# Kernel tuning notes

Hardware: AMD Instinct MI355X
Metric: run time of the kernel (lower is better)

Reference implementation:

```python
import jax, jax.numpy as jnp
import numpy as np

N_NODES = 50000
N_EDGES = 800000
HIDDEN = 128
BN_EPS = 1e-5


def setup_inputs() -> dict:
    key = jax.random.key(0)
    ks = jax.random.split(key, 4)
    x = jax.random.normal(ks[0], (N_NODES, HIDDEN), dtype=jnp.float32)
    edge_index = jax.random.randint(ks[1], (2, N_EDGES), 0, N_NODES, dtype=jnp.int64)
    scale = 1.0 / np.sqrt(HIDDEN)
    W1 = jax.random.normal(ks[2], (HIDDEN, HIDDEN), dtype=jnp.float32) * scale
    b1 = jnp.zeros((HIDDEN,), dtype=jnp.float32)
    W2 = jax.random.normal(ks[3], (HIDDEN, HIDDEN), dtype=jnp.float32) * scale
    b2 = jnp.zeros((HIDDEN,), dtype=jnp.float32)
    gamma = jnp.ones((HIDDEN,), dtype=jnp.float32)
    beta = jnp.zeros((HIDDEN,), dtype=jnp.float32)
    return {"x": x, "edge_index": edge_index, "W1": W1, "b1": b1,
            "W2": W2, "b2": b2, "gamma": gamma, "beta": beta}


def reference(x, edge_index, W1, b1, W2, b2, gamma, beta):
    # GINConv (eps=0): h_i = MLP( x_i + sum_{(j->i) in E} x_j )
    src = edge_index[0]
    dst = edge_index[1]
    agg = jax.ops.segment_sum(x[src], dst, num_segments=x.shape[0])  # [N, H]
    h = x + agg
    # 2-layer MLP: Linear -> ReLU -> Linear
    h = jnp.maximum(h @ W1 + b1, 0.0)
    h = h @ W2 + b2
    # BatchNorm1d over node dimension (training-mode batch statistics)
    mean = jnp.mean(h, axis=0)
    var = jnp.var(h, axis=0)
    h = (h - mean) * jax.lax.rsqrt(var + BN_EPS) * gamma + beta
    # add_activation=False (default): no ReLU. Dropout in eval mode: identity.
    return h
```

## Files before the change

kernel.cpp:

```cpp
#include <hip/hip_runtime.h>

typedef unsigned int u32;
typedef unsigned short u16;
typedef __attribute__((ext_vector_type(8))) short short8;
typedef __attribute__((ext_vector_type(4))) float f32x4;

static constexpr int NN = 50000;
static constexpr int NE = 800000;
static constexpr int HH = 128;
static constexpr int NB1 = (NN + 1023) / 1024;
static constexpr int NBK = 196;
static constexpr int EPB = 8192;
static constexpr int NEB = (NE + EPB - 1) / EPB;

__device__ __forceinline__ u32 bf16r(float f) {
  u32 u = __builtin_bit_cast(u32, f);
  return (u + 0x7FFFu + ((u >> 16) & 1u)) >> 16;
}
__device__ __forceinline__ u32 pk2(float lo, float hi) { return bf16r(lo) | (bf16r(hi) << 16); }
__device__ __forceinline__ float bl(u32 p) { return __builtin_bit_cast(float, p << 16); }
__device__ __forceinline__ float bh(u32 p) { return __builtin_bit_cast(float, p & 0xFFFF0000u); }

__global__ __launch_bounds__(256) void prep_kernel(const float4* __restrict__ x,
                                                   uint4* __restrict__ x16,
                                                   const float* __restrict__ W1,
                                                   u16* __restrict__ w1t,
                                                   const float* __restrict__ W2,
                                                   u16* __restrict__ w2t,
                                                   float* __restrict__ stats,
                                                   const int* __restrict__ ei,
                                                   int* __restrict__ hist2d) {
  __shared__ int hist[NBK];
  const int b = blockIdx.x, t = threadIdx.x;
  if (b < 3125) {
    const int i = b * 256 + t;
    const float4 a = x[2 * i];
    const float4 c = x[2 * i + 1];
    uint4 o;
    o.x = pk2(a.x, a.y);
    o.y = pk2(a.z, a.w);
    o.z = pk2(c.x, c.y);
    o.w = pk2(c.z, c.w);
    x16[i] = o;
  } else if (b < 3189) {
    const int o = (b - 3125) * 256 + t;
    const int n = o >> 7, k = o & 127;
    w1t[o] = (u16)bf16r(W1[k * 128 + n]);
  } else if (b < 3253) {
    const int o = (b - 3189) * 256 + t;
    const int n = o >> 7, k = o & 127;
    w2t[o] = (u16)bf16r(W2[k * 128 + n]);
  } else if (b == 3253) {
    stats[t] = 0.f;
  } else {
    const int hb = b - 3254;
    for (int i = t; i < NBK; i += 256) hist[i] = 0;
    __syncthreads();
    const int e0 = hb * EPB;
    const int e1 = min(e0 + EPB, NE);
    for (int e = e0 + t; e < e1; e += 256) atomicAdd(&hist[ei[NE + e] >> 8], 1);
    __syncthreads();
    for (int i = t; i < NBK; i += 256) hist2d[hb * NBK + i] = hist[i];
  }
}

__global__ __launch_bounds__(256) void ph3_kernel(const int* __restrict__ ei,
                                                  const int* __restrict__ hist2d,
                                                  u32* __restrict__ packed) {
  __shared__ int cur[NBK];
  __shared__ int tot[256];
  const int b = blockIdx.x, t = threadIdx.x;
  int total = 0, partial = 0;
  if (t < NBK) {
    for (int bb = 0; bb < NEB; ++bb) {
      const int v = hist2d[bb * NBK + t];
      total += v;
      if (bb < b) partial += v;
    }
  }
  tot[t] = total;
  __syncthreads();
  for (int off = 1; off < 256; off <<= 1) {
    const int add = (t >= off) ? tot[t - off] : 0;
    __syncthreads();
    tot[t] += add;
    __syncthreads();
  }
  if (t < NBK) cur[t] = (t ? tot[t - 1] : 0) + partial;
  __syncthreads();
  const int e0 = b * EPB;
  const int e1 = min(e0 + EPB, NE);
  for (int e = e0 + t; e < e1; e += 256) {
    const int s = ei[e];
    const int d = ei[NE + e];
    const int pos = atomicAdd(&cur[d >> 8], 1);
    packed[pos] = (u32)s | ((u32)(d & 255) << 16);
  }
}

__global__ __launch_bounds__(256) void ph4_kernel(const int* __restrict__ hist2d,
                                                  const u32* __restrict__ packed,
                                                  int* __restrict__ offs,
                                                  int* __restrict__ srcl) {
  __shared__ int hist[256];
  __shared__ int scn[256];
  __shared__ int sb[2];
  const int b = blockIdx.x, t = threadIdx.x;
  int total = 0;
  if (t < NBK)
    for (int bb = 0; bb < NEB; ++bb) total += hist2d[bb * NBK + t];
  scn[t] = total;
  __syncthreads();
  for (int off = 1; off < 256; off <<= 1) {
    const int add = (t >= off) ? scn[t - off] : 0;
    __syncthreads();
    scn[t] += add;
    __syncthreads();
  }
  if (t == b) {
    sb[0] = b ? scn[b - 1] : 0;
    sb[1] = scn[b];
  }
  __syncthreads();
  const int base = sb[0];
  const int cnt = sb[1] - base;

  hist[t] = 0;
  __syncthreads();
  for (int i = t; i < cnt; i += 256) atomicAdd(&hist[packed[base + i] >> 16], 1);
  __syncthreads();
  scn[t] = hist[t];
  __syncthreads();
  for (int off = 1; off < 256; off <<= 1) {
    const int add = (t >= off) ? scn[t - off] : 0;
    __syncthreads();
    scn[t] += add;
    __syncthreads();
  }
  const int excl = t ? scn[t - 1] : 0;
  const int node = b * 256 + t;
  if (node < NN) offs[node] = base + excl;
  if (b == NBK - 1 && t == 0) offs[NN] = NE;
  __syncthreads();
  hist[t] = excl;
  __syncthreads();
  for (int i = t; i < cnt; i += 256) {
    const u32 p = packed[base + i];
    const int r = atomicAdd(&hist[p >> 16], 1);
    srcl[base + r] = (int)(p & 0xFFFFu);
  }
}

__global__ __launch_bounds__(256) void gather16_kernel(const u32* __restrict__ x16,
                                                       const int* __restrict__ offs,
                                                       const int* __restrict__ srcl,
                                                       u32* __restrict__ h0) {
  const int qw = (blockIdx.x * 256 + threadIdx.x) >> 4;
  const int l16 = threadIdx.x & 15;
  const int nqw = gridDim.x * 16;
  const uint4* x4 = reinterpret_cast<const uint4*>(x16);
  for (int node = qw; node < NN; node += nqw) {
    const uint4 sv = x4[(size_t)node * 16 + l16];
    float a0 = bl(sv.x), a1 = bh(sv.x), a2 = bl(sv.y), a3 = bh(sv.y);
    float a4 = bl(sv.z), a5 = bh(sv.z), a6 = bl(sv.w), a7 = bh(sv.w);
    const int beg = offs[node], end = offs[node + 1];
    int e = beg;
    for (; e + 8 <= end; e += 8) {
      int s[8];
#pragma unroll
      for (int j = 0; j < 8; ++j) s[j] = srcl[e + j];
      uint4 v[8];
#pragma unroll
      for (int j = 0; j < 8; ++j) v[j] = x4[(size_t)s[j] * 16 + l16];
#pragma unroll
      for (int j = 0; j < 8; ++j) {
        a0 += bl(v[j].x); a1 += bh(v[j].x);
        a2 += bl(v[j].y); a3 += bh(v[j].y);
        a4 += bl(v[j].z); a5 += bh(v[j].z);
        a6 += bl(v[j].w); a7 += bh(v[j].w);
      }
    }
    for (; e < end; ++e) {
      const uint4 v = x4[(size_t)srcl[e] * 16 + l16];
      a0 += bl(v.x); a1 += bh(v.x);
      a2 += bl(v.y); a3 += bh(v.y);
      a4 += bl(v.z); a5 += bh(v.z);
      a6 += bl(v.w); a7 += bh(v.w);
    }
    uint4 o;
    o.x = pk2(a0, a1);
    o.y = pk2(a2, a3);
    o.z = pk2(a4, a5);
    o.w = pk2(a6, a7);
    reinterpret_cast<uint4*>(h0)[(size_t)node * 16 + l16] = o;
  }
}

__global__ __launch_bounds__(256) void fused_mlp_kernel(const u16* __restrict__ h0,
                                                        const u16* __restrict__ w1t,
                                                        const float* __restrict__ b1,
                                                        const u16* __restrict__ w2t,
                                                        const float* __restrict__ b2,
                                                        u32* __restrict__ h2,
                                                        float* __restrict__ stats,
                                                        int nchunk) {
  __shared__ __align__(16) u16 hs[16][136];
  __shared__ float sstats[256];
  const int t = threadIdx.x;
  const int w = t >> 6;
  const int lane = t & 63;
  const int lhi = lane >> 4, llo = lane & 15;
  sstats[t] = 0.f;

  short8 w1f[2][4], w2f[2][4];
  float4 bs1[2], bs2[2];
#pragma unroll
  for (int c = 0; c < 2; ++c) {
    const int ct = 2 * w + c;
#pragma unroll
    for (int kb = 0; kb < 4; ++kb) {
      w1f[c][kb] = *reinterpret_cast<const short8*>(w1t + (size_t)(16 * ct + llo) * 128 + kb * 32 + lhi * 8);
      w2f[c][kb] = *reinterpret_cast<const short8*>(w2t + (size_t)(16 * ct + llo) * 128 + kb * 32 + lhi * 8);
    }
    bs1[c] = *reinterpret_cast<const float4*>(b1 + ct * 16 + lhi * 4);
    bs2[c] = *reinterpret_cast<const float4*>(b2 + ct * 16 + lhi * 4);
  }
  __syncthreads();

  for (int ch = blockIdx.x; ch < nchunk; ch += gridDim.x) {
    const int row0 = ch * 16;

    const u16* arow = h0 + (size_t)(row0 + llo) * 128;
    short8 afr[4];
#pragma unroll
    for (int kb = 0; kb < 4; ++kb)
      afr[kb] = *reinterpret_cast<const short8*>(arow + kb * 32 + lhi * 8);

    f32x4 acc0 = {0.f, 0.f, 0.f, 0.f};
    f32x4 acc1 = {0.f, 0.f, 0.f, 0.f};
#pragma unroll
    for (int kb = 0; kb < 4; ++kb) {
      acc0 = __builtin_amdgcn_mfma_f32_16x16x32_bf16(w1f[0][kb], afr[kb], acc0, 0, 0, 0);
      acc1 = __builtin_amdgcn_mfma_f32_16x16x32_bf16(w1f[1][kb], afr[kb], acc1, 0, 0, 0);
    }

#pragma unroll
    for (int c = 0; c < 2; ++c) {
      const int ct = 2 * w + c;
      const f32x4 a = c ? acc1 : acc0;
      const float4 bb = c ? bs1[1] : bs1[0];
      const float v0 = fmaxf(a[0] + bb.x, 0.f);
      const float v1 = fmaxf(a[1] + bb.y, 0.f);
      const float v2 = fmaxf(a[2] + bb.z, 0.f);
      const float v3 = fmaxf(a[3] + bb.w, 0.f);
      u32* dst = reinterpret_cast<u32*>(&hs[llo][ct * 16 + lhi * 4]);
      dst[0] = pk2(v0, v1);
      dst[1] = pk2(v2, v3);
    }
    __syncthreads();

    short8 af2[4];
#pragma unroll
    for (int kb = 0; kb < 4; ++kb)
      af2[kb] = *reinterpret_cast<const short8*>(&hs[llo][kb * 32 + lhi * 8]);

    f32x4 dcc0 = {0.f, 0.f, 0.f, 0.f};
    f32x4 dcc1 = {0.f, 0.f, 0.f, 0.f};
#pragma unroll
    for (int kb = 0; kb < 4; ++kb) {
      dcc0 = __builtin_amdgcn_mfma_f32_16x16x32_bf16(w2f[0][kb], af2[kb], dcc0, 0, 0, 0);
      dcc1 = __builtin_amdgcn_mfma_f32_16x16x32_bf16(w2f[1][kb], af2[kb], dcc1, 0, 0, 0);
    }
    __syncthreads();

#pragma unroll
    for (int c = 0; c < 2; ++c) {
      const int ct = 2 * w + c;
      const f32x4 a = c ? dcc1 : dcc0;
      const float4 bb = c ? bs2[1] : bs2[0];
      float v0 = a[0] + bb.x;
      float v1 = a[1] + bb.y;
      float v2 = a[2] + bb.z;
      float v3 = a[3] + bb.w;
      u32* op = h2 + (size_t)(row0 + llo) * 64 + ct * 8 + lhi * 2;
      op[0] = pk2(v0, v1);
      op[1] = pk2(v2, v3);
      float q0 = v0 * v0, q1 = v1 * v1, q2 = v2 * v2, q3 = v3 * v3;
#pragma unroll
      for (int m = 1; m < 16; m <<= 1) {
        v0 += __shfl_xor(v0, m, 64); v1 += __shfl_xor(v1, m, 64);
        v2 += __shfl_xor(v2, m, 64); v3 += __shfl_xor(v3, m, 64);
        q0 += __shfl_xor(q0, m, 64); q1 += __shfl_xor(q1, m, 64);
        q2 += __shfl_xor(q2, m, 64); q3 += __shfl_xor(q3, m, 64);
      }
      if (llo == 0) {
        const int cb = ct * 16 + lhi * 4;
        atomicAdd(&sstats[cb + 0], v0); atomicAdd(&sstats[cb + 1], v1);
        atomicAdd(&sstats[cb + 2], v2); atomicAdd(&sstats[cb + 3], v3);
        atomicAdd(&sstats[128 + cb + 0], q0); atomicAdd(&sstats[128 + cb + 1], q1);
        atomicAdd(&sstats[128 + cb + 2], q2); atomicAdd(&sstats[128 + cb + 3], q3);
      }
    }
  }
  __syncthreads();
  atomicAdd(&stats[t], sstats[t]);
}

__global__ __launch_bounds__(256) void bn16_kernel(const u32* __restrict__ h2,
                                                   const float* __restrict__ stats,
                                                   const float* __restrict__ gamma,
                                                   const float* __restrict__ beta,
                                                   float* __restrict__ out, float invn) {
  __shared__ float scale_s[128], shift_s[128];
  const int t = threadIdx.x;
  if (t < 128) {
    const float mean = stats[t] * invn;
    float var = fmaf(-mean, mean, stats[128 + t] * invn);
    var = fmaxf(var, 0.f);
    const float rs = rsqrtf(var + 1e-5f);
    const float sc = gamma[t] * rs;
    scale_s[t] = sc;
    shift_s[t] = fmaf(-mean, sc, beta[t]);
  }
  __syncthreads();
  int i = blockIdx.x * 256 + t;
  const int stride = gridDim.x * 256;
  for (; i < NN * 64; i += stride) {
    const int c = (i & 63) * 2;
    const u32 p = h2[i];
    float2 o;
    o.x = fmaf(bl(p), scale_s[c + 0], shift_s[c + 0]);
    o.y = fmaf(bh(p), scale_s[c + 1], shift_s[c + 1]);
    *reinterpret_cast<float2*>(out + 2 * (size_t)i) = o;
  }
}

__global__ void zero_stats_kernel(float* __restrict__ stats) { stats[threadIdx.x] = 0.f; }

__global__ __launch_bounds__(256) void zero_int_kernel(int* __restrict__ p, int n) {
  int i = blockIdx.x * blockDim.x + threadIdx.x;
  const int stride = gridDim.x * blockDim.x;
  for (; i < n; i += stride) p[i] = 0;
}

__global__ __launch_bounds__(256) void count_kernel(const int* __restrict__ ei,
                                                    int* __restrict__ cnt) {
  const int e = blockIdx.x * blockDim.x + threadIdx.x;
  if (e < NE) atomicAdd(&cnt[ei[NE + e]], 1);
}

__global__ __launch_bounds__(256) void scan1_kernel(const int* __restrict__ cnt,
                                                    int* __restrict__ offs,
                                                    int* __restrict__ partials) {
  __shared__ int tsum[256];
  const int b = blockIdx.x, t = threadIdx.x;
  const int base = b * 1024 + t * 4;
  int v[4];
  int s = 0;
#pragma unroll
  for (int j = 0; j < 4; ++j) {
    const int idx = base + j;
    v[j] = (idx < NN) ? cnt[idx] : 0;
    s += v[j];
  }
  tsum[t] = s;
  __syncthreads();
#pragma unroll
  for (int off = 1; off < 256; off <<= 1) {
    const int add = (t >= off) ? tsum[t - off] : 0;
    __syncthreads();
    tsum[t] += add;
    __syncthreads();
  }
  int excl = (t ? tsum[t - 1] : 0);
#pragma unroll
  for (int j = 0; j < 4; ++j) {
    const int idx = base + j;
    if (idx < NN) offs[idx] = excl;
    excl += v[j];
  }
  if (t == 255) partials[b] = tsum[255];
}

__global__ void scan2_kernel(int* __restrict__ partials, int nb) {
  const int t = threadIdx.x;
  int v = (t < nb) ? partials[t] : 0;
#pragma unroll
  for (int off = 1; off < 64; off <<= 1) {
    const int n = __shfl_up(v, off, 64);
    if (t >= off) v += n;
  }
  int excl = __shfl_up(v, 1, 64);
  if (t == 0) excl = 0;
  if (t < nb) partials[t] = excl;
}

__global__ __launch_bounds__(256) void scan3_kernel(int* __restrict__ offs,
                                                    int* __restrict__ cursor,
                                                    const int* __restrict__ partials) {
  const int b = blockIdx.x;
  const int add = partials[b];
#pragma unroll
  for (int j = 0; j < 4; ++j) {
    const int idx = b * 1024 + threadIdx.x + j * 256;
    if (idx < NN) {
      const int o = offs[idx] + add;
      offs[idx] = o;
      cursor[idx] = o;
    }
  }
  if (b == 0 && threadIdx.x == 0) offs[NN] = NE;
}

__global__ __launch_bounds__(256) void fill_kernel(const int* __restrict__ ei,
                                                   int* __restrict__ cursor,
                                                   int* __restrict__ srcl) {
  const int e = blockIdx.x * blockDim.x + threadIdx.x;
  if (e >= NE) return;
  const int s = ei[e];
  const int d = ei[NE + e];
  const int pos = atomicAdd(&cursor[d], 1);
  srcl[pos] = s;
}

__global__ __launch_bounds__(256) void gather_kernel(const float* __restrict__ x,
                                                     const int* __restrict__ offs,
                                                     const int* __restrict__ srcl,
                                                     float* __restrict__ out) {
  const int wave = (blockIdx.x * 256 + threadIdx.x) >> 6;
  const int lane = threadIdx.x & 63;
  const int nwaves = gridDim.x * 4;
  for (int node = wave; node < NN; node += nwaves) {
    float2 acc = *reinterpret_cast<const float2*>(x + (size_t)node * HH + lane * 2);
    const int beg = offs[node], end = offs[node + 1];
    for (int e = beg; e < end; ++e) {
      const int s = srcl[e];
      const float2 v = *reinterpret_cast<const float2*>(x + (size_t)s * HH + lane * 2);
      acc.x += v.x;
      acc.y += v.y;
    }
    *reinterpret_cast<float2*>(out + (size_t)node * HH + lane * 2) = acc;
  }
}

__global__ __launch_bounds__(256) void copy_x_kernel(const float4* __restrict__ x,
                                                     float4* __restrict__ h, int n4) {
  int i = blockIdx.x * blockDim.x + threadIdx.x;
  const int stride = gridDim.x * blockDim.x;
  for (; i < n4; i += stride) h[i] = x[i];
}

__global__ __launch_bounds__(256) void scatter_kernel(const float* __restrict__ x,
                                                      const int* __restrict__ ei,
                                                      float* __restrict__ h) {
  const long long tid = (long long)blockIdx.x * blockDim.x + threadIdx.x;
  const int e = (int)(tid >> 5);
  if (e >= NE) return;
  const int c = (int)(tid & 31);
  const int s = ei[e];
  const int d = ei[NE + e];
  const float4 v = *reinterpret_cast<const float4*>(x + (size_t)s * HH + c * 4);
  float* dp = h + (size_t)d * HH + c * 4;
  atomicAdd(dp + 0, v.x);
  atomicAdd(dp + 1, v.y);
  atomicAdd(dp + 2, v.z);
  atomicAdd(dp + 3, v.w);
}

template <bool RELU>
__global__ __launch_bounds__(256, 2) void gemm128_kernel(const float* in,
                                                         const float* __restrict__ W,
                                                         const float* __restrict__ bias,
                                                         float* out,
                                                         int nrows, int nchunks) {
  __shared__ float Ws[128][128];
  __shared__ float rows_s[32][128];
  const int t = threadIdx.x;
  for (int i = t; i < 128 * 128 / 4; i += 256) {
    reinterpret_cast<float4*>(&Ws[0][0])[i] = reinterpret_cast<const float4*>(W)[i];
  }
  const int col4 = (t & 31) * 4;
  const int rowg = (t >> 5) * 4;
  const float4 b4 = *reinterpret_cast<const float4*>(bias + col4);

  for (int chunk = blockIdx.x; chunk < nchunks; chunk += gridDim.x) {
    const int row0 = chunk * 32;
    __syncthreads();
    for (int i = t; i < 1024; i += 256) {
      const int rr = i >> 5, cc = (i & 31) * 4;
      const int grow = row0 + rr;
      float4 v = make_float4(0.f, 0.f, 0.f, 0.f);
      if (grow < nrows) v = *reinterpret_cast<const float4*>(in + (size_t)grow * HH + cc);
      *reinterpret_cast<float4*>(&rows_s[rr][cc]) = v;
    }
    __syncthreads();

    float acc[4][4] = {};
#pragma unroll 4
    for (int k = 0; k < 128; k += 4) {
      float4 a[4];
#pragma unroll
      for (int r = 0; r < 4; ++r) a[r] = *reinterpret_cast<const float4*>(&rows_s[rowg + r][k]);
#pragma unroll
      for (int kk = 0; kk < 4; ++kk) {
        const float4 wv = *reinterpret_cast<const float4*>(&Ws[k + kk][col4]);
#pragma unroll
        for (int r = 0; r < 4; ++r) {
          const float av = (&a[r].x)[kk];
          acc[r][0] = fmaf(av, wv.x, acc[r][0]);
          acc[r][1] = fmaf(av, wv.y, acc[r][1]);
          acc[r][2] = fmaf(av, wv.z, acc[r][2]);
          acc[r][3] = fmaf(av, wv.w, acc[r][3]);
        }
      }
    }

#pragma unroll
    for (int r = 0; r < 4; ++r) {
      const int grow = row0 + rowg + r;
      if (grow < nrows) {
        float4 o;
        o.x = acc[r][0] + b4.x;
        o.y = acc[r][1] + b4.y;
        o.z = acc[r][2] + b4.z;
        o.w = acc[r][3] + b4.w;
        if (RELU) {
          o.x = fmaxf(o.x, 0.f); o.y = fmaxf(o.y, 0.f);
          o.z = fmaxf(o.z, 0.f); o.w = fmaxf(o.w, 0.f);
        }
        *reinterpret_cast<float4*>(out + (size_t)grow * HH + col4) = o;
      }
    }
  }
}

__global__ __launch_bounds__(256) void col_stats_kernel(const float* __restrict__ h,
                                                        float* __restrict__ stats, int nrows) {
  __shared__ float ssum[256], ssq[256];
  const int t = threadIdx.x;
  const int col = t & 127;
  const int half = t >> 7;
  float s = 0.f, q = 0.f;
  for (int r = blockIdx.x * 2 + half; r < nrows; r += gridDim.x * 2) {
    const float v = h[(size_t)r * HH + col];
    s += v;
    q = fmaf(v, v, q);
  }
  ssum[t] = s;
  ssq[t] = q;
  __syncthreads();
  if (t < 128) {
    atomicAdd(&stats[col], ssum[t] + ssum[t + 128]);
    atomicAdd(&stats[128 + col], ssq[t] + ssq[t + 128]);
  }
}

__global__ __launch_bounds__(256) void bn_apply_kernel(float* __restrict__ h,
                                                       const float* __restrict__ stats,
                                                       const float* __restrict__ gamma,
                                                       const float* __restrict__ beta,
                                                       int n4, float invn) {
  __shared__ float scale_s[128], shift_s[128];
  const int t = threadIdx.x;
  if (t < 128) {
    const float mean = stats[t] * invn;
    float var = fmaf(-mean, mean, stats[128 + t] * invn);
    var = fmaxf(var, 0.f);
    const float rs = rsqrtf(var + 1e-5f);
    const float sc = gamma[t] * rs;
    scale_s[t] = sc;
    shift_s[t] = fmaf(-mean, sc, beta[t]);
  }
  __syncthreads();
  float4* h4 = reinterpret_cast<float4*>(h);
  int i = blockIdx.x * blockDim.x + threadIdx.x;
  const int stride = gridDim.x * blockDim.x;
  for (; i < n4; i += stride) {
    const int c = (i & 31) * 4;
    float4 v = h4[i];
    v.x = fmaf(v.x, scale_s[c + 0], shift_s[c + 0]);
    v.y = fmaf(v.y, scale_s[c + 1], shift_s[c + 1]);
    v.z = fmaf(v.z, scale_s[c + 2], shift_s[c + 2]);
    v.w = fmaf(v.w, scale_s[c + 3], shift_s[c + 3]);
    h4[i] = v;
  }
}

extern "C" void kernel_launch(void* const* d_in, const int* in_sizes, int n_in,
                              void* d_out, int out_size, void* d_ws, size_t ws_size,
                              hipStream_t stream) {
  const float* x = (const float*)d_in[0];
  const int* ei = (const int*)d_in[1];
  const float* W1 = (const float*)d_in[2];
  const float* b1 = (const float*)d_in[3];
  const float* W2 = (const float*)d_in[4];
  const float* b2 = (const float*)d_in[5];
  const float* gamma = (const float*)d_in[6];
  const float* beta = (const float*)d_in[7];
  float* out = (float*)d_out;

  auto AL = [](size_t v) { return (v + 255) & ~(size_t)255; };
  const size_t offs_b = AL((size_t)(NN + 1) * 4);
  const size_t srcl_b = AL((size_t)NE * 4);
  const size_t packed_b = AL((size_t)NE * 4);
  const size_t h2d_b = AL((size_t)NEB * NBK * 4);
  const size_t stats_b = AL(256 * 4);
  const size_t x16_b = AL((size_t)NN * HH * 2);
  const size_t wt_b = AL((size_t)128 * 128 * 2);
  const size_t need_A = offs_b + srcl_b + packed_b + h2d_b + stats_b + x16_b + 2 * wt_b;

  const size_t cnt_b = AL((size_t)NN * 4);
  const size_t part_b = AL(64 * 4);
  const size_t need_B = offs_b + cnt_b + part_b + srcl_b + stats_b;

  if (ws_size >= need_A) {
    char* p = (char*)d_ws;
    int* offs = (int*)p;       p += offs_b;
    int* srcl = (int*)p;       p += srcl_b;
    u32* packed = (u32*)p;     p += packed_b;
    int* hist2d = (int*)p;     p += h2d_b;
    float* stats = (float*)p;  p += stats_b;
    u16* x16 = (u16*)p;        p += x16_b;
    u16* w1t = (u16*)p;        p += wt_b;
    u16* w2t = (u16*)p;

    prep_kernel<<<3254 + NEB, 256, 0, stream>>>((const float4*)x, (uint4*)x16, W1, w1t,
                                                W2, w2t, stats, ei, hist2d);
    ph3_kernel<<<NEB, 256, 0, stream>>>(ei, hist2d, packed);
    ph4_kernel<<<NBK, 256, 0, stream>>>(hist2d, packed, offs, srcl);

    gather16_kernel<<<2048, 256, 0, stream>>>((const u32*)x16, offs, srcl, (u32*)d_out);

    const int nchunk = NN / 16;
    u32* h2 = (u32*)x16;
    fused_mlp_kernel<<<512, 256, 0, stream>>>((const u16*)d_out, w1t, b1, w2t, b2,
                                              h2, stats, nchunk);
    bn16_kernel<<<2048, 256, 0, stream>>>(h2, stats, gamma, beta, out, 1.0f / NN);
  } else if (ws_size >= need_B) {
    char* p = (char*)d_ws;
    int* offs = (int*)p;      p += offs_b;
    int* cnt = (int*)p;       p += cnt_b;
    int* partials = (int*)p;  p += part_b;
    int* srcl = (int*)p;      p += srcl_b;
    float* stats = (float*)p;

    zero_int_kernel<<<64, 256, 0, stream>>>(cnt, NN);
    count_kernel<<<(NE + 255) / 256, 256, 0, stream>>>(ei, cnt);
    scan1_kernel<<<NB1, 256, 0, stream>>>(cnt, offs, partials);
    scan2_kernel<<<1, 64, 0, stream>>>(partials, NB1);
    scan3_kernel<<<NB1, 256, 0, stream>>>(offs, cnt, partials);
    fill_kernel<<<(NE + 255) / 256, 256, 0, stream>>>(ei, cnt, srcl);
    gather_kernel<<<1024, 256, 0, stream>>>(x, offs, srcl, out);

    zero_stats_kernel<<<1, 256, 0, stream>>>(stats);
    const int nchunks = (NN + 31) / 32;
    gemm128_kernel<true><<<512, 256, 0, stream>>>(out, W1, b1, out, NN, nchunks);
    gemm128_kernel<false><<<512, 256, 0, stream>>>(out, W2, b2, out, NN, nchunks);
    col_stats_kernel<<<1024, 256, 0, stream>>>(out, stats, NN);
    bn_apply_kernel<<<2048, 256, 0, stream>>>(out, stats, gamma, beta, NN * HH / 4, 1.0f / NN);
  } else {
    float* stats = (float*)d_ws;
    copy_x_kernel<<<2048, 256, 0, stream>>>((const float4*)x, (float4*)out, NN * HH / 4);
    const long long sthreads = (long long)NE * 32;
    scatter_kernel<<<(int)((sthreads + 255) / 256), 256, 0, stream>>>(x, ei, out);
    zero_stats_kernel<<<1, 256, 0, stream>>>(stats);
    const int nchunks = (NN + 31) / 32;
    gemm128_kernel<true><<<512, 256, 0, stream>>>(out, W1, b1, out, NN, nchunks);
    gemm128_kernel<false><<<512, 256, 0, stream>>>(out, W2, b2, out, NN, nchunks);
    col_stats_kernel<<<1024, 256, 0, stream>>>(out, stats, NN);
    bn_apply_kernel<<<2048, 256, 0, stream>>>(out, stats, gamma, beta, NN * HH / 4, 1.0f / NN);
  }
}
```

Measured before the change: 131.5 us.

## Fuse per-bucket CSR sort into gather kernel using shared-memory source lists

The per-bucket counting sort that built global offs/srcl arrays is merged with the gather into one sortgather kernel. Each of 8 blocks per 256-node bucket re-sorts the bucket's packed edges into shared memory and then gathers its 32 nodes. Bucket offsets are now emitted by ph3 instead of being recomputed from hist2d. This removes one kernel launch and the global write and read of srcl/offs. In exchange, every block repeats the bucket sort, and any bucket with more than SCAP edges would silently drop entries.

```diff
diff --git a/kernel.cpp b/kernel.cpp
--- a/kernel.cpp
+++ b/kernel.cpp
@@ -12,6 +12,8 @@
 static constexpr int NBK = 196;
 static constexpr int EPB = 8192;
 static constexpr int NEB = (NE + EPB - 1) / EPB;
+static constexpr int KSPLIT = 8;
+static constexpr int SCAP = 6144;
 
 __device__ __forceinline__ u32 bf16r(float f) {
   u32 u = __builtin_bit_cast(u32, f);
@@ -66,7 +68,8 @@
 
 __global__ __launch_bounds__(256) void ph3_kernel(const int* __restrict__ ei,
                                                   const int* __restrict__ hist2d,
-                                                  u32* __restrict__ packed) {
+                                                  u32* __restrict__ packed,
+                                                  int* __restrict__ boffs) {
   __shared__ int cur[NBK];
   __shared__ int tot[256];
   const int b = blockIdx.x, t = threadIdx.x;
@@ -86,7 +89,12 @@
     tot[t] += add;
     __syncthreads();
   }
-  if (t < NBK) cur[t] = (t ? tot[t - 1] : 0) + partial;
+  const int excl = t ? tot[t - 1] : 0;
+  if (t < NBK) cur[t] = excl + partial;
+  if (b == 0) {
+    if (t < NBK) boffs[t] = excl;
+    if (t == 0) boffs[NBK] = NE;
+  }
   __syncthreads();
   const int e0 = b * EPB;
   const int e1 = min(e0 + EPB, NE);
@@ -98,18 +106,25 @@
   }
 }
 
-__global__ __launch_bounds__(256) void ph4_kernel(const int* __restrict__ hist2d,
-                                                  const u32* __restrict__ packed,
-                                                  int* __restrict__ offs,
-                                                  int* __restrict__ srcl) {
+__global__ __launch_bounds__(256) void sortgather_kernel(const u32* __restrict__ packed,
+                                                         const int* __restrict__ boffs,
+                                                         const u32* __restrict__ x16,
+                                                         u32* __restrict__ h0) {
   __shared__ int hist[256];
   __shared__ int scn[256];
-  __shared__ int sb[2];
-  const int b = blockIdx.x, t = threadIdx.x;
-  int total = 0;
-  if (t < NBK)
-    for (int bb = 0; bb < NEB; ++bb) total += hist2d[bb * NBK + t];
-  scn[t] = total;
+  __shared__ int soffs[257];
+  __shared__ int ssrc[SCAP];
+  const int bkt = blockIdx.x >> 3;
+  const int part = blockIdx.x & 7;
+  const int t = threadIdx.x;
+  const int base = boffs[bkt];
+  const int cnt = boffs[bkt + 1] - base;
+
+  hist[t] = 0;
+  __syncthreads();
+  for (int i = t; i < cnt; i += 256) atomicAdd(&hist[packed[base + i] >> 16], 1);
+  __syncthreads();
+  scn[t] = hist[t];
   __syncthreads();
   for (int off = 1; off < 256; off <<= 1) {
     const int add = (t >= off) ? scn[t - off] : 0;
@@ -117,58 +132,33 @@
     scn[t] += add;
     __syncthreads();
   }
-  if (t == b) {
-    sb[0] = b ? scn[b - 1] : 0;
-    sb[1] = scn[b];
-  }
-  __syncthreads();
-  const int base = sb[0];
-  const int cnt = sb[1] - base;
-
-  hist[t] = 0;
-  __syncthreads();
-  for (int i = t; i < cnt; i += 256) atomicAdd(&hist[packed[base + i] >> 16], 1);
-  __syncthreads();
-  scn[t] = hist[t];
-  __syncthreads();
-  for (int off = 1; off < 256; off <<= 1) {
-    const int add = (t >= off) ? scn[t - off] : 0;
-    __syncthreads();
-    scn[t] += add;
-    __syncthreads();
-  }
   const int excl = t ? scn[t - 1] : 0;
-  const int node = b * 256 + t;
-  if (node < NN) offs[node] = base + excl;
-  if (b == NBK - 1 && t == 0) offs[NN] = NE;
-  __syncthreads();
+  soffs[t] = excl;
+  if (t == 255) soffs[256] = scn[255];
   hist[t] = excl;
   __syncthreads();
   for (int i = t; i < cnt; i += 256) {
     const u32 p = packed[base + i];
     const int r = atomicAdd(&hist[p >> 16], 1);
-    srcl[base + r] = (int)(p & 0xFFFFu);
-  }
-}
-
-__global__ __launch_bounds__(256) void gather16_kernel(const u32* __restrict__ x16,
-                                                       const int* __restrict__ offs,
-                                                       const int* __restrict__ srcl,
-                                                       u32* __restrict__ h0) {
-  const int qw = (blockIdx.x * 256 + threadIdx.x) >> 4;
-  const int l16 = threadIdx.x & 15;
-  const int nqw = gridDim.x * 16;
+    if (r < SCAP) ssrc[r] = (int)(p & 0xFFFFu);
+  }
+  __syncthreads();
+
+  const int qw = t >> 4;
+  const int l16 = t & 15;
   const uint4* x4 = reinterpret_cast<const uint4*>(x16);
-  for (int node = qw; node < NN; node += nqw) {
-    const uint4 sv = x4[(size_t)node * 16 + l16];
+  for (int ln = part * 32 + qw; ln < part * 32 + 32; ln += 16) {
+    const int g = bkt * 256 + ln;
+    if (g >= NN) continue;
+    const uint4 sv = x4[(size_t)g * 16 + l16];
     float a0 = bl(sv.x), a1 = bh(sv.x), a2 = bl(sv.y), a3 = bh(sv.y);
     float a4 = bl(sv.z), a5 = bh(sv.z), a6 = bl(sv.w), a7 = bh(sv.w);
-    const int beg = offs[node], end = offs[node + 1];
+    const int beg = soffs[ln], end = soffs[ln + 1];
     int e = beg;
     for (; e + 8 <= end; e += 8) {
       int s[8];
 #pragma unroll
-      for (int j = 0; j < 8; ++j) s[j] = srcl[e + j];
+      for (int j = 0; j < 8; ++j) s[j] = ssrc[e + j];
       uint4 v[8];
 #pragma unroll
       for (int j = 0; j < 8; ++j) v[j] = x4[(size_t)s[j] * 16 + l16];
@@ -181,7 +171,7 @@
       }
     }
     for (; e < end; ++e) {
-      const uint4 v = x4[(size_t)srcl[e] * 16 + l16];
+      const uint4 v = x4[(size_t)ssrc[e] * 16 + l16];
       a0 += bl(v.x); a1 += bh(v.x);
       a2 += bl(v.y); a3 += bh(v.y);
       a4 += bl(v.z); a5 += bh(v.z);
@@ -192,7 +182,7 @@
     o.y = pk2(a2, a3);
     o.z = pk2(a4, a5);
     o.w = pk2(a6, a7);
-    reinterpret_cast<uint4*>(h0)[(size_t)node * 16 + l16] = o;
+    reinterpret_cast<uint4*>(h0)[(size_t)g * 16 + l16] = o;
   }
 }
 
@@ -600,25 +590,25 @@
   float* out = (float*)d_out;
 
   auto AL = [](size_t v) { return (v + 255) & ~(size_t)255; };
-  const size_t offs_b = AL((size_t)(NN + 1) * 4);
-  const size_t srcl_b = AL((size_t)NE * 4);
   const size_t packed_b = AL((size_t)NE * 4);
   const size_t h2d_b = AL((size_t)NEB * NBK * 4);
+  const size_t boffs_b = AL((size_t)(NBK + 1) * 4);
   const size_t stats_b = AL(256 * 4);
   const size_t x16_b = AL((size_t)NN * HH * 2);
   const size_t wt_b = AL((size_t)128 * 128 * 2);
-  const size_t need_A = offs_b + srcl_b + packed_b + h2d_b + stats_b + x16_b + 2 * wt_b;
-
+  const size_t need_A = packed_b + h2d_b + boffs_b + stats_b + x16_b + 2 * wt_b;
+
+  const size_t offs_b = AL((size_t)(NN + 1) * 4);
   const size_t cnt_b = AL((size_t)NN * 4);
   const size_t part_b = AL(64 * 4);
+  const size_t srcl_b = AL((size_t)NE * 4);
   const size_t need_B = offs_b + cnt_b + part_b + srcl_b + stats_b;
 
   if (ws_size >= need_A) {
     char* p = (char*)d_ws;
-    int* offs = (int*)p;       p += offs_b;
-    int* srcl = (int*)p;       p += srcl_b;
     u32* packed = (u32*)p;     p += packed_b;
     int* hist2d = (int*)p;     p += h2d_b;
+    int* boffs = (int*)p;      p += boffs_b;
     float* stats = (float*)p;  p += stats_b;
     u16* x16 = (u16*)p;        p += x16_b;
     u16* w1t = (u16*)p;        p += wt_b;
@@ -626,11 +616,9 @@
 
     prep_kernel<<<3254 + NEB, 256, 0, stream>>>((const float4*)x, (uint4*)x16, W1, w1t,
                                                 W2, w2t, stats, ei, hist2d);
-    ph3_kernel<<<NEB, 256, 0, stream>>>(ei, hist2d, packed);
-    ph4_kernel<<<NBK, 256, 0, stream>>>(hist2d, packed, offs, srcl);
-
-    gather16_kernel<<<2048, 256, 0, stream>>>((const u32*)x16, offs, srcl, (u32*)d_out);
-
+    ph3_kernel<<<NEB, 256, 0, stream>>>(ei, hist2d, packed, boffs);
+    sortgather_kernel<<<NBK * KSPLIT, 256, 0, stream>>>(packed, boffs, (const u32*)x16,
+                                                        (u32*)d_out);
     const int nchunk = NN / 16;
     u32* h2 = (u32*)x16;
     fused_mlp_kernel<<<512, 256, 0, stream>>>((const u16*)d_out, w1t, b1, w2t, b2,
```

After: 133.6 us. Within noise of the previous version (+1.6%).
